# Kernel tuning notes

Measured on AMD Instinct MI355X. Metric: run time of the kernel, lower is better.

## Reference

```python
import jax, jax.numpy as jnp
import numpy as np

SEQ, BATCH, IN_DIM, HID = 1024, 512, 128, 128


def _linear_params(key, fan_in, fan_out):
    # matches torch nn.Linear default init: U(-1/sqrt(fan_in), 1/sqrt(fan_in))
    s = 1.0 / np.sqrt(fan_in)
    k1, k2 = jax.random.split(key)
    W = jax.random.uniform(k1, (fan_in, fan_out), minval=-s, maxval=s, dtype=jnp.float32)
    b = jax.random.uniform(k2, (fan_out,), minval=-s, maxval=s, dtype=jnp.float32)
    return W, b


def setup_inputs() -> dict:
    key = jax.random.key(0)
    ks = jax.random.split(key, 5)
    inputs = jax.random.normal(ks[0], (SEQ, BATCH, IN_DIM), dtype=jnp.float32)
    Wf, bf = _linear_params(ks[1], IN_DIM + HID, HID)
    Wi, bi = _linear_params(ks[2], IN_DIM + HID, HID)
    Wg, bg = _linear_params(ks[3], IN_DIM + HID, HID)
    Wo, bo = _linear_params(ks[4], IN_DIM + HID, HID)
    return {"inputs": inputs, "Wf": Wf, "bf": bf, "Wi": Wi, "bi": bi,
            "Wg": Wg, "bg": bg, "Wo": Wo, "bo": bo}


def reference(inputs, Wf, bf, Wi, bi, Wg, bg, Wo, bo):
    # inputs: [seq, batch, in_dim] (time-major, matches torch unbind(dim=0))
    B = inputs.shape[1]
    H = Wf.shape[1]
    h0 = jnp.zeros((B, H), dtype=inputs.dtype)
    c0 = jnp.zeros((B, H), dtype=inputs.dtype)

    def step(carry, x):
        hx, cx = carry
        comb = jnp.concatenate([x, hx], axis=1)  # [B, in_dim+H]
        f_lin = comb @ Wf + bf
        i_lin = comb @ Wi + bi
        g = jnp.tanh(comb @ Wg + bg)
        o = jax.nn.sigmoid(comb @ Wo + bo)
        # Quantum sampler, closed form:
        #  - RX(theta)|0> has <Z> = cos(theta)
        #  - CNOT chain over f-wires pulls Z_j back to Z_0...Z_j -> cumprod of cos
        #  - i-wires untouched by CNOTs -> plain cos
        #  probs = (<Z> + 1) / 2
        f = (jnp.cumprod(jnp.cos(f_lin), axis=1) + 1.0) * 0.5
        i = (jnp.cos(i_lin) + 1.0) * 0.5
        cx_new = f * cx + i * g
        hx_new = o * jnp.tanh(cx_new)
        return (hx_new, cx_new), hx_new

    (hx, cx), outputs = jax.lax.scan(step, (h0, c0), inputs)
    return outputs, hx, cx
```

## Files before the change

kernel.cpp:

```cpp
#include <hip/hip_runtime.h>

#define SEQ   1024
#define BATCH 512
#define HID   128

typedef __attribute__((ext_vector_type(8))) short  short8v;
typedef __attribute__((ext_vector_type(4))) float  float4v;
typedef __attribute__((ext_vector_type(2))) float  float2v;

__device__ __forceinline__ unsigned short f2bf(float f) {
    union { float f; unsigned u; } v; v.f = f;
    return (unsigned short)((v.u + 0x7fffu + ((v.u >> 16) & 1u)) >> 16);
}
__device__ __forceinline__ float fast_cos(float x) {
    return __builtin_amdgcn_cosf(x * 0.15915494309189535f);
}
__device__ __forceinline__ float fast_sigmoid(float x) {
    return __builtin_amdgcn_rcpf(1.0f + __builtin_amdgcn_exp2f(-1.4426950408889634f * x));
}
__device__ __forceinline__ float fast_tanh(float x) {
    return 1.0f - 2.0f * __builtin_amdgcn_rcpf(1.0f + __builtin_amdgcn_exp2f(2.8853900817779268f * x));
}
template<int CTRL, int RM>
__device__ __forceinline__ float dpp1(float v) {
    union { float f; int i; } s, o, r;
    s.f = v; o.f = 1.0f;
    r.i = __builtin_amdgcn_update_dpp(o.i, s.i, CTRL, RM, 0xf, false);
    return r.f;
}
#define BAR() do { asm volatile("s_waitcnt lgkmcnt(0)" ::: "memory");  \
                   __builtin_amdgcn_s_barrier();                       \
                   __builtin_amdgcn_sched_barrier(0); } while (0)

__device__ __forceinline__ void fscan(float a, float b, int kg,
                                      float& Fa, float& Fb) {
    float Sa = a, Sb = b;
    Sa *= dpp1<0x111, 0xf>(Sa);  Sb *= dpp1<0x111, 0xf>(Sb);
    Sa *= dpp1<0x112, 0xf>(Sa);  Sb *= dpp1<0x112, 0xf>(Sb);
    Sa *= dpp1<0x114, 0xf>(Sa);  Sb *= dpp1<0x114, 0xf>(Sb);
    Sa *= dpp1<0x118, 0xf>(Sa);  Sb *= dpp1<0x118, 0xf>(Sb);
    const float T0a = __shfl(Sa, 15), T0b = __shfl(Sb, 15);
    const float T1a = __shfl(Sa, 31), T1b = __shfl(Sb, 31);
    const float T2a = __shfl(Sa, 47), T2b = __shfl(Sb, 47);
    const float Taown = __shfl(Sa, kg * 16 + 15);
    const float p0 = T0a * T0b, p1 = T1a * T1b, p2 = T2a * T2b;
    const float rp = (kg == 0) ? 1.f : (kg == 1) ? p0
                   : (kg == 2) ? p0 * p1 : p0 * p1 * p2;
    Fa = rp * Sa;
    Fb = rp * Taown * Sb;
}

__global__ __launch_bounds__(512, 1) void qlstm_fused(
    const float* __restrict__ X,
    const float* __restrict__ Wf, const float* __restrict__ bfp,
    const float* __restrict__ Wi, const float* __restrict__ bip,
    const float* __restrict__ Wg, const float* __restrict__ bgp,
    const float* __restrict__ Wo, const float* __restrict__ bop,
    float* __restrict__ out)
{
    __shared__ alignas(16) float zring[8][4][HID][2];
    __shared__ alignas(16) float gact[2][4][HID];
    __shared__ alignas(8)  unsigned short h_bf[2][HID];
    __shared__ alignas(8)  unsigned short x_bf[2][HID];

    const int tid = threadIdx.x, lane = tid & 63, wid = tid >> 6;
    const int l15 = lane & 15, kg = lane >> 4;
    const int b0 = blockIdx.x * 2;
    const bool prod = (wid >= 4);
    const int g = wid & 3;
    const float* Wsel = (g == 0) ? Wf : (g == 1) ? Wi : (g == 2) ? Wg : Wo;
    const float* bsel = (g == 0) ? bfp : (g == 1) ? bip : (g == 2) ? bgp : bop;

    short8v bw[8][4];
    {
        const int kbase = prod ? 0 : 128;
        #pragma unroll
        for (int n = 0; n < 8; ++n) {
            const int col = n * 16 + l15;
            #pragma unroll
            for (int ks = 0; ks < 4; ++ks) {
                const int k0 = kbase + ks * 32 + kg * 8;
                short8v a;
                #pragma unroll
                for (int j = 0; j < 8; ++j)
                    a[j] = (short)f2bf(Wsel[(size_t)(k0 + j) * HID + col]);
                bw[n][ks] = a;
            }
        }
    }
    float biasr[8];
    #pragma unroll
    for (int n = 0; n < 8; ++n) biasr[n] = prod ? bsel[n * 16 + l15] : 0.f;

    if (tid < 128) ((unsigned*)h_bf)[tid] = 0u;

    const int crow = wid >> 1;
    const int ccol = (wid & 1) * 64 + lane;
    float c_reg = 0.f, h_last = 0.f;
    const int ca0 = kg * 32 + l15;

    #pragma unroll 1
    for (int p = 0; p < 4; ++p) {
        if (wid == 4) {
            float4v xv0 = *(const float4v*)(X + ((size_t)p * BATCH + b0) * HID + lane * 4);
            unsigned* dst = (unsigned*)&x_bf[lane >> 5][(lane & 31) * 4];
            dst[0] = (unsigned)f2bf(xv0[0]) | ((unsigned)f2bf(xv0[1]) << 16);
            dst[1] = (unsigned)f2bf(xv0[2]) | ((unsigned)f2bf(xv0[3]) << 16);
        }
        BAR();
        if (prod) {
            short8v ax[4];
            #pragma unroll
            for (int ks = 0; ks < 4; ++ks)
                ax[ks] = *(const short8v*)&x_bf[l15 & 1][ks * 32 + kg * 8];
            float4v acc[8];
            #pragma unroll
            for (int n = 0; n < 8; ++n)
                #pragma unroll
                for (int j = 0; j < 4; ++j) acc[n][j] = biasr[n];
            #pragma unroll
            for (int ks = 0; ks < 4; ++ks)
                #pragma unroll
                for (int n = 0; n < 8; ++n)
                    acc[n] = __builtin_amdgcn_mfma_f32_16x16x32_bf16(ax[ks], bw[n][ks], acc[n], 0, 0, 0);
            if (kg == 0) {
                #pragma unroll
                for (int n = 0; n < 8; ++n) {
                    float2v zz; zz[0] = acc[n][0]; zz[1] = acc[n][1];
                    *(float2v*)&zring[p][g][n * 16 + l15][0] = zz;
                }
            }
        }
        BAR();
    }
    if (wid == 4) {
        float4v xv0 = *(const float4v*)(X + ((size_t)4 * BATCH + b0) * HID + lane * 4);
        unsigned* dst = (unsigned*)&x_bf[lane >> 5][(lane & 31) * 4];
        dst[0] = (unsigned)f2bf(xv0[0]) | ((unsigned)f2bf(xv0[1]) << 16);
        dst[1] = (unsigned)f2bf(xv0[2]) | ((unsigned)f2bf(xv0[3]) << 16);
    }
    BAR();
    float4v xv;
    if (wid == 4) xv = *(const float4v*)(X + ((size_t)5 * BATCH + b0) * HID + lane * 4);

    for (int t = 0; t < SEQ; ++t) {
        const int slot = t & 7;

        if (!prod) {
            short8v ah[4];
            #pragma unroll
            for (int ks = 0; ks < 4; ++ks)
                ah[ks] = *(const short8v*)&h_bf[l15 & 1][ks * 32 + kg * 8];

            float4v acc[8];
            #pragma unroll
            for (int n = 0; n < 8; ++n)
                #pragma unroll
                for (int j = 0; j < 4; ++j) acc[n][j] = 0.f;

            __builtin_amdgcn_s_setprio(1);
            #pragma unroll
            for (int ks = 0; ks < 4; ++ks)
                #pragma unroll
                for (int n = 0; n < 8; ++n)
                    acc[n] = __builtin_amdgcn_mfma_f32_16x16x32_bf16(ah[ks], bw[n][ks], acc[n], 0, 0, 0);
            __builtin_amdgcn_s_setprio(0);

            float2v zr0 = *(const float2v*)&zring[slot][g][ca0][0];
            float2v zr1 = *(const float2v*)&zring[slot][g][ca0 + 16][0];

            float s0r0 = (kg == 0) ? acc[0][0] : (kg == 1) ? acc[2][0]
                       : (kg == 2) ? acc[4][0] : acc[6][0];
            float s0r1 = (kg == 0) ? acc[0][1] : (kg == 1) ? acc[2][1]
                       : (kg == 2) ? acc[4][1] : acc[6][1];
            float s1r0 = (kg == 0) ? acc[1][0] : (kg == 1) ? acc[3][0]
                       : (kg == 2) ? acc[5][0] : acc[7][0];
            float s1r1 = (kg == 0) ? acc[1][1] : (kg == 1) ? acc[3][1]
                       : (kg == 2) ? acc[5][1] : acc[7][1];
            s0r0 += zr0[0]; s0r1 += zr0[1];
            s1r0 += zr1[0]; s1r1 += zr1[1];

            float v00, v01, v10, v11;
            if (g == 0) {
                float Fa0, Fb0, Fa1, Fb1;
                fscan(fast_cos(s0r0), fast_cos(s1r0), kg, Fa0, Fb0);
                fscan(fast_cos(s0r1), fast_cos(s1r1), kg, Fa1, Fb1);
                v00 = (Fa0 + 1.f) * 0.5f; v01 = (Fb0 + 1.f) * 0.5f;
                v10 = (Fa1 + 1.f) * 0.5f; v11 = (Fb1 + 1.f) * 0.5f;
            } else if (g == 1) {
                v00 = (fast_cos(s0r0) + 1.f) * .5f; v01 = (fast_cos(s1r0) + 1.f) * .5f;
                v10 = (fast_cos(s0r1) + 1.f) * .5f; v11 = (fast_cos(s1r1) + 1.f) * .5f;
            } else if (g == 2) {
                v00 = fast_tanh(s0r0); v01 = fast_tanh(s1r0);
                v10 = fast_tanh(s0r1); v11 = fast_tanh(s1r1);
            } else {
                v00 = fast_sigmoid(s0r0); v01 = fast_sigmoid(s1r0);
                v10 = fast_sigmoid(s0r1); v11 = fast_sigmoid(s1r1);
            }
            gact[0][g][ca0]      = v00;
            gact[0][g][ca0 + 16] = v01;
            gact[1][g][ca0]      = v10;
            gact[1][g][ca0 + 16] = v11;
        } else if (t + 4 < SEQ) {
            short8v ax[4];
            #pragma unroll
            for (int ks = 0; ks < 4; ++ks)
                ax[ks] = *(const short8v*)&x_bf[l15 & 1][ks * 32 + kg * 8];
            float4v acc[8];
            #pragma unroll
            for (int n = 0; n < 8; ++n)
                #pragma unroll
                for (int j = 0; j < 4; ++j) acc[n][j] = biasr[n];
            #pragma unroll
            for (int ks = 0; ks < 4; ++ks)
                #pragma unroll
                for (int n = 0; n < 8; ++n)
                    acc[n] = __builtin_amdgcn_mfma_f32_16x16x32_bf16(ax[ks], bw[n][ks], acc[n], 0, 0, 0);
            if (kg == 0) {
                const int sp = (t + 4) & 7;
                #pragma unroll
                for (int n = 0; n < 8; ++n) {
                    float2v zz; zz[0] = acc[n][0]; zz[1] = acc[n][1];
                    *(float2v*)&zring[sp][g][n * 16 + l15][0] = zz;
                }
            }
        }
        BAR();

        if (!prod) {
            const float f  = gact[crow][0][ccol];
            const float i_ = gact[crow][1][ccol];
            const float g_ = gact[crow][2][ccol];
            const float o_ = gact[crow][3][ccol];
            const float cn = fmaf(f, c_reg, i_ * g_);
            const float hn = o_ * fast_tanh(cn);
            c_reg = cn; h_last = hn;
            h_bf[crow][ccol] = f2bf(hn);
            out[((size_t)t * BATCH + b0 + crow) * HID + ccol] = hn;
        } else if (wid == 4) {
            if (t + 5 < SEQ) {
                unsigned* dst = (unsigned*)&x_bf[lane >> 5][(lane & 31) * 4];
                dst[0] = (unsigned)f2bf(xv[0]) | ((unsigned)f2bf(xv[1]) << 16);
                dst[1] = (unsigned)f2bf(xv[2]) | ((unsigned)f2bf(xv[3]) << 16);
                if (t + 6 < SEQ)
                    xv = *(const float4v*)(X + ((size_t)(t + 6) * BATCH + b0) * HID + lane * 4);
            }
        }
        BAR();
    }

    if (!prod) {
        const size_t base = (size_t)SEQ * BATCH * HID;
        const size_t ro = (size_t)(b0 + crow) * HID + ccol;
        out[base + ro] = h_last;
        out[base + (size_t)BATCH * HID + ro] = c_reg;
    }
}

extern "C" void kernel_launch(void* const* d_in, const int* in_sizes, int n_in,
                              void* d_out, int out_size, void* d_ws, size_t ws_size,
                              hipStream_t stream) {
    const float* X  = (const float*)d_in[0];
    const float* Wf = (const float*)d_in[1];
    const float* bf = (const float*)d_in[2];
    const float* Wi = (const float*)d_in[3];
    const float* bi = (const float*)d_in[4];
    const float* Wg = (const float*)d_in[5];
    const float* bg = (const float*)d_in[6];
    const float* Wo = (const float*)d_in[7];
    const float* bo = (const float*)d_in[8];
    float* out = (float*)d_out;
    (void)d_ws; (void)ws_size;

    qlstm_fused<<<BATCH / 2, 512, 0, stream>>>(
        X, Wf, bf, Wi, bi, Wg, bg, Wo, bo, out);
}
```

Baseline: 1.111 ms.

## Merge producer waves into recurrent waves with batched 8-step input projection

The kernel drops from 8 waves to 4. Each wave now holds both the input and hidden weight halves in registers and computes one 16-row tile of the input projection for 8 future timesteps alongside its recurrent MFMA work each step. Input rows are staged 8 timesteps at a time into a swizzled bf16 LDS window, and precomputed projections are stored as packed bf16 in a swizzled 16-slot ring. This removes the separate producer waves and their per-step contention, but it doubles register pressure per wave, adds extra MFMAs to the critical per-step path, and lowers precision of the input projection to bf16.

Result: slower. 1.620 ms (+45.8%).

```diff
diff --git a/kernel.cpp b/kernel.cpp
--- a/kernel.cpp
+++ b/kernel.cpp
@@ -4,13 +4,20 @@
 #define BATCH 512
 #define HID   128
 
-typedef __attribute__((ext_vector_type(8))) short  short8v;
-typedef __attribute__((ext_vector_type(4))) float  float4v;
-typedef __attribute__((ext_vector_type(2))) float  float2v;
+typedef __attribute__((ext_vector_type(8))) short          short8v;
+typedef __attribute__((ext_vector_type(4))) float          float4v;
+typedef __attribute__((ext_vector_type(8))) unsigned short ushort8v;
 
 __device__ __forceinline__ unsigned short f2bf(float f) {
     union { float f; unsigned u; } v; v.f = f;
     return (unsigned short)((v.u + 0x7fffu + ((v.u >> 16) & 1u)) >> 16);
+}
+__device__ __forceinline__ float bf2f(unsigned short u) {
+    union { unsigned u; float f; } v; v.u = ((unsigned)u) << 16;
+    return v.f;
+}
+__device__ __forceinline__ unsigned packbf(float a, float b) {
+    return (unsigned)f2bf(a) | ((unsigned)f2bf(b) << 16);
 }
 __device__ __forceinline__ float fast_cos(float x) {
     return __builtin_amdgcn_cosf(x * 0.15915494309189535f);
@@ -50,7 +57,14 @@
     Fb = rp * Taown * Sb;
 }
 
-__global__ __launch_bounds__(512, 1) void qlstm_fused(
+__device__ __forceinline__ int zswz(int slot, int g, int c) {
+    return slot * 512 + g * 128 + (c ^ ((c >> 5) << 4) ^ ((slot & 2) << 3));
+}
+__device__ __forceinline__ int gswz(int row, int g, int c) {
+    return row * 512 + g * 128 + (c ^ ((c >> 5) << 4));
+}
+
+__global__ __launch_bounds__(256, 1) void qlstm_fused(
     const float* __restrict__ X,
     const float* __restrict__ Wf, const float* __restrict__ bfp,
     const float* __restrict__ Wi, const float* __restrict__ bip,
@@ -58,203 +72,218 @@
     const float* __restrict__ Wo, const float* __restrict__ bop,
     float* __restrict__ out)
 {
-    __shared__ alignas(16) float zring[8][4][HID][2];
-    __shared__ alignas(16) float gact[2][4][HID];
-    __shared__ alignas(8)  unsigned short h_bf[2][HID];
-    __shared__ alignas(8)  unsigned short x_bf[2][HID];
+    __shared__ unsigned zr_lds[16 * 4 * 128];
+    __shared__ float    ga_lds[2 * 4 * 128];
+    __shared__ alignas(16) unsigned short h_bf[2][HID];
+    __shared__ alignas(16) unsigned short x_win[2][16][HID];
 
     const int tid = threadIdx.x, lane = tid & 63, wid = tid >> 6;
     const int l15 = lane & 15, kg = lane >> 4;
     const int b0 = blockIdx.x * 2;
-    const bool prod = (wid >= 4);
-    const int g = wid & 3;
+    const int g = wid;
     const float* Wsel = (g == 0) ? Wf : (g == 1) ? Wi : (g == 2) ? Wg : Wo;
     const float* bsel = (g == 0) ? bfp : (g == 1) ? bip : (g == 2) ? bgp : bop;
 
-    short8v bw[8][4];
-    {
-        const int kbase = prod ? 0 : 128;
-        #pragma unroll
-        for (int n = 0; n < 8; ++n) {
-            const int col = n * 16 + l15;
-            #pragma unroll
-            for (int ks = 0; ks < 4; ++ks) {
-                const int k0 = kbase + ks * 32 + kg * 8;
-                short8v a;
-                #pragma unroll
-                for (int j = 0; j < 8; ++j)
-                    a[j] = (short)f2bf(Wsel[(size_t)(k0 + j) * HID + col]);
-                bw[n][ks] = a;
+    short8v bwh[8][4], bwx[8][4];
+    #pragma unroll
+    for (int n = 0; n < 8; ++n) {
+        const int col = n * 16 + l15;
+        #pragma unroll
+        for (int ks = 0; ks < 4; ++ks) {
+            short8v wh, wx;
+            #pragma unroll
+            for (int j = 0; j < 8; ++j) {
+                const int k = ks * 32 + kg * 8 + j;
+                wx[j] = (short)f2bf(Wsel[(size_t)k * HID + col]);
+                wh[j] = (short)f2bf(Wsel[(size_t)(128 + k) * HID + col]);
             }
+            bwx[n][ks] = wx;
+            bwh[n][ks] = wh;
         }
     }
     float biasr[8];
     #pragma unroll
-    for (int n = 0; n < 8; ++n) biasr[n] = prod ? bsel[n * 16 + l15] : 0.f;
+    for (int n = 0; n < 8; ++n) biasr[n] = bsel[n * 16 + l15];
 
     if (tid < 128) ((unsigned*)h_bf)[tid] = 0u;
 
     const int crow = wid >> 1;
     const int ccol = (wid & 1) * 64 + lane;
+    const int ca0  = kg * 32 + l15;
     float c_reg = 0.f, h_last = 0.f;
-    const int ca0 = kg * 32 + l15;
+
+    const int sm  = tid >> 4;
+    const int sbl = tid & 15;
+    const size_t xrow_off = ((size_t)(b0 + (sm & 1))) * HID + sbl * 8;
+    const int xw_off = (sbl * 16) ^ ((sm & 7) << 4);
+    const int xsw = (l15 & 7) << 4;
+
+#define STAGE_XWIN(buf, s0) do {                                                   \
+    const float* xp_ = X + ((size_t)((s0) + (sm >> 1)) * BATCH) * HID + xrow_off;  \
+    float4v a_ = *(const float4v*)xp_;                                             \
+    float4v b_ = *(const float4v*)(xp_ + 4);                                       \
+    ushort8v o_;                                                                   \
+    o_[0]=f2bf(a_[0]); o_[1]=f2bf(a_[1]); o_[2]=f2bf(a_[2]); o_[3]=f2bf(a_[3]);    \
+    o_[4]=f2bf(b_[0]); o_[5]=f2bf(b_[1]); o_[6]=f2bf(b_[2]); o_[7]=f2bf(b_[3]);    \
+    *(ushort8v*)((char*)&x_win[buf][sm][0] + xw_off) = o_;                         \
+} while (0)
+
+#define LOAD_AX(buf) do {                                                          \
+    const char* xb_ = (const char*)&x_win[buf][0][0] + l15 * 256;                  \
+    ax[0] = *(const short8v*)(xb_ + ((      kg * 16) ^ xsw));                      \
+    ax[1] = *(const short8v*)(xb_ + (( 64 + kg * 16) ^ xsw));                      \
+    ax[2] = *(const short8v*)(xb_ + ((128 + kg * 16) ^ xsw));                      \
+    ax[3] = *(const short8v*)(xb_ + ((192 + kg * 16) ^ xsw));                      \
+} while (0)
+
+#define XTILE(N) do {                                                              \
+    float4v xa_;                                                                   \
+    xa_[0] = biasr[N]; xa_[1] = biasr[N]; xa_[2] = biasr[N]; xa_[3] = biasr[N];    \
+    xa_ = __builtin_amdgcn_mfma_f32_16x16x32_bf16(ax[0], bwx[N][0], xa_, 0, 0, 0); \
+    xa_ = __builtin_amdgcn_mfma_f32_16x16x32_bf16(ax[1], bwx[N][1], xa_, 0, 0, 0); \
+    xa_ = __builtin_amdgcn_mfma_f32_16x16x32_bf16(ax[2], bwx[N][2], xa_, 0, 0, 0); \
+    xa_ = __builtin_amdgcn_mfma_f32_16x16x32_bf16(ax[3], bwx[N][3], xa_, 0, 0, 0); \
+    const int se_ = (bnext + kg * 2) & 15;                                         \
+    const int cs_ = (N) * 16 + l15;                                                \
+    zr_lds[zswz(se_,     g, cs_)] = packbf(xa_[0], xa_[1]);                        \
+    zr_lds[zswz(se_ + 1, g, cs_)] = packbf(xa_[2], xa_[3]);                        \
+} while (0)
+
+    short8v ax[4];
+    float4v xg0 = {}, xg1 = {};
+
+    STAGE_XWIN(0, 0);
+    STAGE_XWIN(1, 8);
+    BAR();
+    LOAD_AX(0);
+    {
+        float4v pacc[8];
+        #pragma unroll
+        for (int n = 0; n < 8; ++n)
+            #pragma unroll
+            for (int j = 0; j < 4; ++j) pacc[n][j] = biasr[n];
+        #pragma unroll
+        for (int ks = 0; ks < 4; ++ks)
+            #pragma unroll
+            for (int n = 0; n < 8; ++n)
+                pacc[n] = __builtin_amdgcn_mfma_f32_16x16x32_bf16(ax[ks], bwx[n][ks], pacc[n], 0, 0, 0);
+        #pragma unroll
+        for (int n = 0; n < 8; ++n) {
+            const int se_ = kg * 2;
+            const int cs_ = n * 16 + l15;
+            zr_lds[zswz(se_,     g, cs_)] = packbf(pacc[n][0], pacc[n][1]);
+            zr_lds[zswz(se_ + 1, g, cs_)] = packbf(pacc[n][2], pacc[n][3]);
+        }
+    }
+    BAR();
 
     #pragma unroll 1
-    for (int p = 0; p < 4; ++p) {
-        if (wid == 4) {
-            float4v xv0 = *(const float4v*)(X + ((size_t)p * BATCH + b0) * HID + lane * 4);
-            unsigned* dst = (unsigned*)&x_bf[lane >> 5][(lane & 31) * 4];
-            dst[0] = (unsigned)f2bf(xv0[0]) | ((unsigned)f2bf(xv0[1]) << 16);
-            dst[1] = (unsigned)f2bf(xv0[2]) | ((unsigned)f2bf(xv0[3]) << 16);
-        }
+    for (int t = 0; t < SEQ; ++t) {
+        const int w = t & 7;
+        const int W = t >> 3;
+        const int bnext = (t & ~7) + 8;
+
+        const unsigned zp0 = zr_lds[zswz(t & 15, g, ca0)];
+        const unsigned zp1 = zr_lds[zswz(t & 15, g, ca0 + 16)];
+        short8v ah[4];
+        #pragma unroll
+        for (int ks = 0; ks < 4; ++ks)
+            ah[ks] = *(const short8v*)&h_bf[l15 & 1][ks * 32 + kg * 8];
+
+        if (w == 0) {
+            if (bnext < SEQ) LOAD_AX((W + 1) & 1);
+            if (bnext + 8 < SEQ) {
+                const float* xp = X + ((size_t)(bnext + 8 + (sm >> 1)) * BATCH) * HID + xrow_off;
+                xg0 = *(const float4v*)xp;
+                xg1 = *(const float4v*)(xp + 4);
+            }
+        }
+
+        float4v acc[8];
+        #pragma unroll
+        for (int n = 0; n < 8; ++n)
+            #pragma unroll
+            for (int j = 0; j < 4; ++j) acc[n][j] = 0.f;
+        #pragma unroll
+        for (int ks = 0; ks < 4; ++ks)
+            #pragma unroll
+            for (int n = 0; n < 8; ++n)
+                acc[n] = __builtin_amdgcn_mfma_f32_16x16x32_bf16(ah[ks], bwh[n][ks], acc[n], 0, 0, 0);
+
+        if (bnext < SEQ) {
+            switch (w) {
+                case 0: XTILE(0); break;
+                case 1: XTILE(1); break;
+                case 2: XTILE(2); break;
+                case 3: XTILE(3); break;
+                case 4: XTILE(4); break;
+                case 5: XTILE(5); break;
+                case 6: XTILE(6); break;
+                default: XTILE(7); break;
+            }
+        }
+
+        float s0r0 = ((kg == 0) ? acc[0][0] : (kg == 1) ? acc[2][0]
+                    : (kg == 2) ? acc[4][0] : acc[6][0]) + bf2f((unsigned short)(zp0 & 0xffffu));
+        float s0r1 = ((kg == 0) ? acc[0][1] : (kg == 1) ? acc[2][1]
+                    : (kg == 2) ? acc[4][1] : acc[6][1]) + bf2f((unsigned short)(zp0 >> 16));
+        float s1r0 = ((kg == 0) ? acc[1][0] : (kg == 1) ? acc[3][0]
+                    : (kg == 2) ? acc[5][0] : acc[7][0]) + bf2f((unsigned short)(zp1 & 0xffffu));
+        float s1r1 = ((kg == 0) ? acc[1][1] : (kg == 1) ? acc[3][1]
+                    : (kg == 2) ? acc[5][1] : acc[7][1]) + bf2f((unsigned short)(zp1 >> 16));
+
+        float v00, v01, v10, v11;
+        if (g == 0) {
+            float Fa0, Fb0, Fa1, Fb1;
+            fscan(fast_cos(s0r0), fast_cos(s1r0), kg, Fa0, Fb0);
+            fscan(fast_cos(s0r1), fast_cos(s1r1), kg, Fa1, Fb1);
+            v00 = (Fa0 + 1.f) * 0.5f; v01 = (Fb0 + 1.f) * 0.5f;
+            v10 = (Fa1 + 1.f) * 0.5f; v11 = (Fb1 + 1.f) * 0.5f;
+        } else if (g == 1) {
+            v00 = (fast_cos(s0r0) + 1.f) * .5f; v01 = (fast_cos(s1r0) + 1.f) * .5f;
+            v10 = (fast_cos(s0r1) + 1.f) * .5f; v11 = (fast_cos(s1r1) + 1.f) * .5f;
+        } else if (g == 2) {
+            v00 = fast_tanh(s0r0); v01 = fast_tanh(s1r0);
+            v10 = fast_tanh(s0r1); v11 = fast_tanh(s1r1);
+        } else {
+            v00 = fast_sigmoid(s0r0); v01 = fast_sigmoid(s1r0);
+            v10 = fast_sigmoid(s0r1); v11 = fast_sigmoid(s1r1);
+        }
+        ga_lds[gswz(0, g, ca0)]      = v00;
+        ga_lds[gswz(0, g, ca0 + 16)] = v01;
+        ga_lds[gswz(1, g, ca0)]      = v10;
+        ga_lds[gswz(1, g, ca0 + 16)] = v11;
+
         BAR();
-        if (prod) {
-            short8v ax[4];
-            #pragma unroll
-            for (int ks = 0; ks < 4; ++ks)
-                ax[ks] = *(const short8v*)&x_bf[l15 & 1][ks * 32 + kg * 8];
-            float4v acc[8];
-            #pragma unroll
-            for (int n = 0; n < 8; ++n)
-                #pragma unroll
-                for (int j = 0; j < 4; ++j) acc[n][j] = biasr[n];
-            #pragma unroll
-            for (int ks = 0; ks < 4; ++ks)
-                #pragma unroll
-                for (int n = 0; n < 8; ++n)
-                    acc[n] = __builtin_amdgcn_mfma_f32_16x16x32_bf16(ax[ks], bw[n][ks], acc[n], 0, 0, 0);
-            if (kg == 0) {
-                #pragma unroll
-                for (int n = 0; n < 8; ++n) {
-                    float2v zz; zz[0] = acc[n][0]; zz[1] = acc[n][1];
-                    *(float2v*)&zring[p][g][n * 16 + l15][0] = zz;
-                }
-            }
+
+        const float fv = ga_lds[gswz(crow, 0, ccol)];
+        const float iv = ga_lds[gswz(crow, 1, ccol)];
+        const float gv = ga_lds[gswz(crow, 2, ccol)];
+        const float ov = ga_lds[gswz(crow, 3, ccol)];
+        const float cn = fmaf(fv, c_reg, iv * gv);
+        const float hn = ov * fast_tanh(cn);
+        c_reg = cn; h_last = hn;
+        h_bf[crow][ccol] = f2bf(hn);
+        out[((size_t)t * BATCH + b0 + crow) * HID + ccol] = hn;
+
+        if (w == 4 && bnext + 8 < SEQ) {
+            ushort8v o_;
+            o_[0]=f2bf(xg0[0]); o_[1]=f2bf(xg0[1]); o_[2]=f2bf(xg0[2]); o_[3]=f2bf(xg0[3]);
+            o_[4]=f2bf(xg1[0]); o_[5]=f2bf(xg1[1]); o_[6]=f2bf(xg1[2]); o_[7]=f2bf(xg1[3]);
+            *(ushort8v*)((char*)&x_win[W & 1][sm][0] + xw_off) = o_;
         }
         BAR();
     }
-    if (wid == 4) {
-        float4v xv0 = *(const float4v*)(X + ((size_t)4 * BATCH + b0) * HID + lane * 4);
-        unsigned* dst = (unsigned*)&x_bf[lane >> 5][(lane & 31) * 4];
-        dst[0] = (unsigned)f2bf(xv0[0]) | ((unsigned)f2bf(xv0[1]) << 16);
-        dst[1] = (unsigned)f2bf(xv0[2]) | ((unsigned)f2bf(xv0[3]) << 16);
-    }
-    BAR();
-    float4v xv;
-    if (wid == 4) xv = *(const float4v*)(X + ((size_t)5 * BATCH + b0) * HID + lane * 4);
-
-    for (int t = 0; t < SEQ; ++t) {
-        const int slot = t & 7;
-
-        if (!prod) {
-            short8v ah[4];
-            #pragma unroll
-            for (int ks = 0; ks < 4; ++ks)
-                ah[ks] = *(const short8v*)&h_bf[l15 & 1][ks * 32 + kg * 8];
-
-            float4v acc[8];
-            #pragma unroll
-            for (int n = 0; n < 8; ++n)
-                #pragma unroll
-                for (int j = 0; j < 4; ++j) acc[n][j] = 0.f;
-
-            __builtin_amdgcn_s_setprio(1);
-            #pragma unroll
-            for (int ks = 0; ks < 4; ++ks)
-                #pragma unroll
-                for (int n = 0; n < 8; ++n)
-                    acc[n] = __builtin_amdgcn_mfma_f32_16x16x32_bf16(ah[ks], bw[n][ks], acc[n], 0, 0, 0);
-            __builtin_amdgcn_s_setprio(0);
-
-            float2v zr0 = *(const float2v*)&zring[slot][g][ca0][0];
-            float2v zr1 = *(const float2v*)&zring[slot][g][ca0 + 16][0];
-
-            float s0r0 = (kg == 0) ? acc[0][0] : (kg == 1) ? acc[2][0]
-                       : (kg == 2) ? acc[4][0] : acc[6][0];
-            float s0r1 = (kg == 0) ? acc[0][1] : (kg == 1) ? acc[2][1]
-                       : (kg == 2) ? acc[4][1] : acc[6][1];
-            float s1r0 = (kg == 0) ? acc[1][0] : (kg == 1) ? acc[3][0]
-                       : (kg == 2) ? acc[5][0] : acc[7][0];
-            float s1r1 = (kg == 0) ? acc[1][1] : (kg == 1) ? acc[3][1]
-                       : (kg == 2) ? acc[5][1] : acc[7][1];
-            s0r0 += zr0[0]; s0r1 += zr0[1];
-            s1r0 += zr1[0]; s1r1 += zr1[1];
-
-            float v00, v01, v10, v11;
-            if (g == 0) {
-                float Fa0, Fb0, Fa1, Fb1;
-                fscan(fast_cos(s0r0), fast_cos(s1r0), kg, Fa0, Fb0);
-                fscan(fast_cos(s0r1), fast_cos(s1r1), kg, Fa1, Fb1);
-                v00 = (Fa0 + 1.f) * 0.5f; v01 = (Fb0 + 1.f) * 0.5f;
-                v10 = (Fa1 + 1.f) * 0.5f; v11 = (Fb1 + 1.f) * 0.5f;
-            } else if (g == 1) {
-                v00 = (fast_cos(s0r0) + 1.f) * .5f; v01 = (fast_cos(s1r0) + 1.f) * .5f;
-                v10 = (fast_cos(s0r1) + 1.f) * .5f; v11 = (fast_cos(s1r1) + 1.f) * .5f;
-            } else if (g == 2) {
-                v00 = fast_tanh(s0r0); v01 = fast_tanh(s1r0);
-                v10 = fast_tanh(s0r1); v11 = fast_tanh(s1r1);
-            } else {
-                v00 = fast_sigmoid(s0r0); v01 = fast_sigmoid(s1r0);
-                v10 = fast_sigmoid(s0r1); v11 = fast_sigmoid(s1r1);
-            }
-            gact[0][g][ca0]      = v00;
-            gact[0][g][ca0 + 16] = v01;
-            gact[1][g][ca0]      = v10;
-            gact[1][g][ca0 + 16] = v11;
-        } else if (t + 4 < SEQ) {
-            short8v ax[4];
-            #pragma unroll
-            for (int ks = 0; ks < 4; ++ks)
-                ax[ks] = *(const short8v*)&x_bf[l15 & 1][ks * 32 + kg * 8];
-            float4v acc[8];
-            #pragma unroll
-            for (int n = 0; n < 8; ++n)
-                #pragma unroll
-                for (int j = 0; j < 4; ++j) acc[n][j] = biasr[n];
-            #pragma unroll
-            for (int ks = 0; ks < 4; ++ks)
-                #pragma unroll
-                for (int n = 0; n < 8; ++n)
-                    acc[n] = __builtin_amdgcn_mfma_f32_16x16x32_bf16(ax[ks], bw[n][ks], acc[n], 0, 0, 0);
-            if (kg == 0) {
-                const int sp = (t + 4) & 7;
-                #pragma unroll
-                for (int n = 0; n < 8; ++n) {
-                    float2v zz; zz[0] = acc[n][0]; zz[1] = acc[n][1];
-                    *(float2v*)&zring[sp][g][n * 16 + l15][0] = zz;
-                }
-            }
-        }
-        BAR();
-
-        if (!prod) {
-            const float f  = gact[crow][0][ccol];
-            const float i_ = gact[crow][1][ccol];
-            const float g_ = gact[crow][2][ccol];
-            const float o_ = gact[crow][3][ccol];
-            const float cn = fmaf(f, c_reg, i_ * g_);
-            const float hn = o_ * fast_tanh(cn);
-            c_reg = cn; h_last = hn;
-            h_bf[crow][ccol] = f2bf(hn);
-            out[((size_t)t * BATCH + b0 + crow) * HID + ccol] = hn;
-        } else if (wid == 4) {
-            if (t + 5 < SEQ) {
-                unsigned* dst = (unsigned*)&x_bf[lane >> 5][(lane & 31) * 4];
-                dst[0] = (unsigned)f2bf(xv[0]) | ((unsigned)f2bf(xv[1]) << 16);
-                dst[1] = (unsigned)f2bf(xv[2]) | ((unsigned)f2bf(xv[3]) << 16);
-                if (t + 6 < SEQ)
-                    xv = *(const float4v*)(X + ((size_t)(t + 6) * BATCH + b0) * HID + lane * 4);
-            }
-        }
-        BAR();
-    }
-
-    if (!prod) {
+
+    {
         const size_t base = (size_t)SEQ * BATCH * HID;
         const size_t ro = (size_t)(b0 + crow) * HID + ccol;
         out[base + ro] = h_last;
         out[base + (size_t)BATCH * HID + ro] = c_reg;
     }
+#undef STAGE_XWIN
+#undef LOAD_AX
+#undef XTILE
 }
 
 extern "C" void kernel_launch(void* const* d_in, const int* in_sizes, int n_in,
@@ -272,6 +301,6 @@
     float* out = (float*)d_out;
     (void)d_ws; (void)ws_size;
 
-    qlstm_fused<<<BATCH / 2, 512, 0, stream>>>(
+    qlstm_fused<<<BATCH / 2, 256, 0, stream>>>(
         X, Wf, bf, Wi, bi, Wg, bg, Wo, bo, out);
 }
```
